# Performance work log

Measured on AMD Instinct MI355X. Metric: run time of the kernel, lower is better.

The kernel has to match this reference:

```python
import jax, jax.numpy as jnp
import numpy as np

# dims per module source / chosen globals
B, LB = 4, 28            # new frames, buffered frames; M = B+LB = L = 32
DK, DV = 256, 32         # Dk=256 hardcoded; Dv = 4*len_of_lookup+4 with len_of_lookup=7
HS, WS = 64, 64          # H//8, W//8 with H=W=512
LMAX = 32                # memory cap L
TRAIN_SZ = 1000          # log base train_sz
ALPHA = 0.5              # blend coefficient (original inits 0, which zeroes the branch)
# log(L*h*w + h*w, train_sz) / sqrt(Dk)
SCALE = float(np.log(LMAX * HS * WS + HS * WS) / np.log(TRAIN_SZ) / np.sqrt(DK))


def _xavier(key, fan_in, fan_out):
    lim = np.sqrt(6.0 / (fan_in + fan_out))
    return jax.random.uniform(key, (fan_in, fan_out), jnp.float32, -lim, lim)


def setup_inputs() -> dict:
    key = jax.random.key(0)
    ks = jax.random.split(key, 7)
    return {
        "fc": jax.random.normal(ks[0], (B, DK, HS, WS), jnp.float32),
        "fm": jax.random.normal(ks[1], (B, DV, HS, WS), jnp.float32),
        "key_buffer": jax.random.normal(ks[2], (LB, DK, HS, WS), jnp.float32),
        "value_buffer": jax.random.normal(ks[3], (LB, DV, HS, WS), jnp.float32),
        "Q": _xavier(ks[4], DK, DK),
        "K": _xavier(ks[5], DK, DK),
        "V": _xavier(ks[6], DV, DV),
    }


def reference(fc, fm, key_buffer, value_buffer, Q, K, V):
    # matmul = einsum('ijkl,jm->imkl'): per-pixel channel mixing
    q = jnp.einsum('bdhw,de->behw', fc, Q)                      # [B,Dk,h,w]
    k = jnp.concatenate([jnp.einsum('bdhw,de->behw', fc, K), key_buffer], axis=0)    # [M,Dk,h,w]
    v = jnp.concatenate([jnp.einsum('bdhw,de->behw', fm, V), value_buffer], axis=0)  # [M,Dv,h,w]
    # current_batch (=1) < L, so no slicing of k/v on this step
    scores = SCALE * jnp.einsum('bdhw,mdhw->bmhw', q, k)        # [B,M,h,w]
    attn = jax.nn.softmax(scores, axis=-1)                      # NOTE: softmax over width axis, as in source (dim=-1)
    ctx = jnp.einsum('bmhw,mdhw->bdhw', attn, v)                # [B,Dv,h,w]
    return fm + ALPHA * ctx
```

## Files before the change

kernel.cpp:

```cpp
#include <hip/hip_runtime.h>
#include <hip/hip_bf16.h>
#include <cmath>

#define NB 4
#define NM 32
#define DKc 256
#define DVc 32
#define NP 4096

using bf16x8 = __attribute__((ext_vector_type(8))) short;
using f32x4  = __attribute__((ext_vector_type(4))) float;
using f32x2  = __attribute__((ext_vector_type(2))) float;

__device__ __forceinline__ unsigned short f2bf(float f) {
    union { float f; unsigned u; } x; x.f = f;
    unsigned r = 0x7FFFu + ((x.u >> 16) & 1u);
    return (unsigned short)((x.u + r) >> 16);
}

__global__ __launch_bounds__(256) void k_prep(
    const float* __restrict__ fc, unsigned short* __restrict__ fcT,
    const float* __restrict__ Q, unsigned short* __restrict__ WTq,
    const float* __restrict__ K, unsigned short* __restrict__ WTk,
    const float* __restrict__ fm, const float* __restrict__ V, float* __restrict__ vproj) {
    int x = blockIdx.x;
    int t = threadIdx.x;
    if (x < 1056) {
        __shared__ float tile[64][65];
        const float* s; unsigned short* d; int R, C, r0, c0;
        if (x < 1024) {
            int bb = x >> 8, rest = x & 255;
            R = 256; C = 4096;
            r0 = (rest >> 6) * 64; c0 = (rest & 63) * 64;
            s = fc + (long)bb * 256 * 4096; d = fcT + (long)bb * 256 * 4096;
        } else {
            int i = x - 1024;
            int mat = i >> 4, idx = i & 15;
            R = 256; C = 256;
            r0 = (idx >> 2) * 64; c0 = (idx & 3) * 64;
            s = mat ? K : Q; d = mat ? WTk : WTq;
        }
        #pragma unroll
        for (int j = 0; j < 16; ++j) {
            int i = t + 256 * j;
            int r = i >> 6, c = i & 63;
            tile[r][c] = s[(long)(r0 + r) * C + c0 + c];
        }
        __syncthreads();
        #pragma unroll
        for (int j = 0; j < 8; ++j) {
            int i = t + 256 * j;
            int row = i >> 5;
            int pr = i & 31;
            float f0 = tile[2 * pr][row];
            float f1 = tile[2 * pr + 1][row];
            unsigned pack = (unsigned)f2bf(f0) | ((unsigned)f2bf(f1) << 16);
            reinterpret_cast<unsigned*>(d)[(((long)(c0 + row) * R + r0) >> 1) + pr] = pack;
        }
    } else {
        __shared__ float Vl[32][32];
        __shared__ float fml[32][256];
        int i = x - 1056;
        int b = i >> 4, p0 = (i & 15) * 256;
        #pragma unroll
        for (int j = 0; j < 4; ++j) { int ii = t + 256 * j; Vl[ii >> 5][ii & 31] = V[ii]; }
        for (int j = 0; j < 32; ++j) {
            int ii = t + 256 * j;
            int dd = ii >> 8, c = ii & 255;
            fml[dd][c] = fm[((long)b * DVc + dd) * NP + p0 + c];
        }
        __syncthreads();
        float acc[32];
        #pragma unroll
        for (int e = 0; e < 32; ++e) acc[e] = 0.f;
        for (int dd = 0; dd < 32; ++dd) {
            float fv = fml[dd][t];
            #pragma unroll
            for (int e = 0; e < 32; ++e) acc[e] += fv * Vl[dd][e];
        }
        #pragma unroll
        for (int e = 0; e < 32; ++e) vproj[((long)b * DVc + e) * NP + p0 + t] = acc[e];
    }
}

__global__ __launch_bounds__(256) void k_proj(
    const unsigned short* __restrict__ WTq, const unsigned short* __restrict__ WTk,
    const unsigned short* __restrict__ fcT,
    float* __restrict__ qproj, float* __restrict__ kproj) {
    int t = threadIdx.x;
    int wave = t >> 6, lane = t & 63;
    int y = blockIdx.y;
    int b = y & 3, mat = y >> 2;
    int p0 = blockIdx.x * 64;
    int ln = lane & 15, quad = lane >> 4;
    const unsigned short* WT = mat ? WTk : WTq;
    float* dst = mat ? kproj : qproj;
    int e0w = wave * 64;
    const unsigned short* bbase = fcT + ((long)b * NP + p0 + ln) * DKc + quad * 8;
    f32x4 acc[4][4] = {};
    for (int kk = 0; kk < DKc; kk += 32) {
        bf16x8 a[4], bb[4];
        #pragma unroll
        for (int i = 0; i < 4; ++i)
            a[i] = *reinterpret_cast<const bf16x8*>(WT + (long)(e0w + i * 16 + ln) * DKc + quad * 8 + kk);
        #pragma unroll
        for (int j = 0; j < 4; ++j)
            bb[j] = *reinterpret_cast<const bf16x8*>(bbase + (long)j * 16 * DKc + kk);
        #pragma unroll
        for (int i = 0; i < 4; ++i)
            #pragma unroll
            for (int j = 0; j < 4; ++j)
                acc[i][j] = __builtin_amdgcn_mfma_f32_16x16x32_bf16(a[i], bb[j], acc[i][j], 0, 0, 0);
    }
    #pragma unroll
    for (int i = 0; i < 4; ++i)
        #pragma unroll
        for (int j = 0; j < 4; ++j)
            #pragma unroll
            for (int r = 0; r < 4; ++r) {
                int e = e0w + i * 16 + quad * 4 + r, p = p0 + j * 16 + ln;
                dst[((long)b * DKc + e) * NP + p] = acc[i][j][r];
            }
}

__global__ __launch_bounds__(1024) void k_fused(
    const float* __restrict__ qproj, const float* __restrict__ kproj,
    const float* __restrict__ kbuf, const float* __restrict__ vproj,
    const float* __restrict__ vbuf, const float* __restrict__ fm,
    float* __restrict__ out, float scale) {
    __shared__ float smem[256 * 64];
    int t = threadIdx.x;
    int b = blockIdx.x >> 6, hrow = blockIdx.x & 63;
    int p0 = hrow * 64;
    int wave = t >> 6, lane = t & 63;

    {
        const float* qbase = qproj + (long)b * DKc * NP + p0;
        #pragma unroll
        for (int j = 0; j < 16; ++j) {
            int i = t + 1024 * j;
            int e = i >> 6, w = i & 63;
            smem[e * 64 + w] = qbase[(long)e * NP + w];
        }
    }
    __syncthreads();

    float attnw[2];
    {
        const float* kp[2];
        #pragma unroll
        for (int mi = 0; mi < 2; ++mi) {
            int m = wave * 2 + mi;
            kp[mi] = (m < 4 ? kproj + (long)m * DKc * NP : kbuf + (long)(m - 4) * DKc * NP)
                     + p0 + lane;
        }
        float s[2] = {0.f, 0.f};
        for (int e8 = 0; e8 < 256; e8 += 8) {
            float qv[8], kv[8][2];
            #pragma unroll
            for (int u = 0; u < 8; ++u) qv[u] = smem[(e8 + u) * 64 + lane];
            #pragma unroll
            for (int u = 0; u < 8; ++u)
                #pragma unroll
                for (int mi = 0; mi < 2; ++mi)
                    kv[u][mi] = kp[mi][(long)u * NP];
            #pragma unroll
            for (int u = 0; u < 8; ++u)
                #pragma unroll
                for (int mi = 0; mi < 2; ++mi)
                    s[mi] += qv[u] * kv[u][mi];
            #pragma unroll
            for (int mi = 0; mi < 2; ++mi) kp[mi] += 8 * NP;
        }
        #pragma unroll
        for (int mi = 0; mi < 2; ++mi) {
            float x = s[mi] * scale;
            float mx = x;
            #pragma unroll
            for (int d = 1; d < 64; d <<= 1) mx = fmaxf(mx, __shfl_xor(mx, d));
            float ev = __expf(x - mx);
            float sum = ev;
            #pragma unroll
            for (int d = 1; d < 64; d <<= 1) sum += __shfl_xor(sum, d);
            attnw[mi] = ev / sum;
        }
    }
    __syncthreads();
    #pragma unroll
    for (int mi = 0; mi < 2; ++mi)
        smem[(wave * 2 + mi) * 68 + lane] = attnw[mi];
    __syncthreads();

    {
        int dg = t >> 6, w = t & 63;
        float c2[2] = {0.f, 0.f};
        #pragma unroll
        for (int m = 0; m < NM; ++m) {
            float a = smem[m * 68 + w];
            const float* vp = (m < 4 ? vproj + (long)m * DVc * NP : vbuf + (long)(m - 4) * DVc * NP)
                              + (long)(dg * 2) * NP + p0 + w;
            #pragma unroll
            for (int i = 0; i < 2; ++i) c2[i] += a * vp[(long)i * NP];
        }
        #pragma unroll
        for (int i = 0; i < 2; ++i) {
            long gi = ((long)b * DVc + dg * 2 + i) * NP + p0 + w;
            out[gi] = fm[gi] + 0.5f * c2[i];
        }
    }
}

extern "C" void kernel_launch(void* const* d_in, const int* in_sizes, int n_in,
                              void* d_out, int out_size, void* d_ws, size_t ws_size,
                              hipStream_t stream) {
    const float* fc = (const float*)d_in[0];
    const float* fm = (const float*)d_in[1];
    const float* kb = (const float*)d_in[2];
    const float* vb = (const float*)d_in[3];
    const float* Q  = (const float*)d_in[4];
    const float* K  = (const float*)d_in[5];
    const float* V  = (const float*)d_in[6];
    float* out = (float*)d_out;
    char* ws = (char*)d_ws;
    float*          qproj = (float*)(ws);
    float*          kproj = (float*)(ws + 16777216);
    float*          vproj = (float*)(ws + 33554432);
    unsigned short* fcT   = (unsigned short*)(ws + 35651584);
    unsigned short* WTq   = (unsigned short*)(ws + 44040192);
    unsigned short* WTk   = (unsigned short*)(ws + 44171264);
    float scale = (float)(log(135168.0) / log(1000.0) / 16.0);

    hipLaunchKernelGGL(k_prep, dim3(1120), dim3(256), 0, stream,
                       fc, fcT, Q, WTq, K, WTk, fm, V, vproj);
    hipLaunchKernelGGL(k_proj, dim3(64, 8), dim3(256), 0, stream,
                       WTq, WTk, fcT, qproj, kproj);
    hipLaunchKernelGGL(k_fused, dim3(256), dim3(1024), 0, stream,
                       qproj, kproj, kb, vproj, vb, fm, out, scale);
}
```

Before: 252.6 us.

## Vectorize fused attention loads and split reductions across waves; halve proj pixel tile

The fused kernel now loads keys, queries and values as float4 per lane and splits the Dk reduction (and the memory-slot reduction for context) across two wave halves, combining the partial sums through shared memory. This aims to cut global load instruction count and raise memory-level parallelism on the bandwidth-heavy key-buffer read. The projection kernel's pixel tile drops from 64 to 32 with twice the grid, giving more blocks at the cost of reloading weights more often. It adds extra syncs and shared-memory round trips.

```diff
diff --git a/kernel.cpp b/kernel.cpp
--- a/kernel.cpp
+++ b/kernel.cpp
@@ -91,31 +91,31 @@
     int wave = t >> 6, lane = t & 63;
     int y = blockIdx.y;
     int b = y & 3, mat = y >> 2;
-    int p0 = blockIdx.x * 64;
+    int p0 = blockIdx.x * 32;
     int ln = lane & 15, quad = lane >> 4;
     const unsigned short* WT = mat ? WTk : WTq;
     float* dst = mat ? kproj : qproj;
     int e0w = wave * 64;
     const unsigned short* bbase = fcT + ((long)b * NP + p0 + ln) * DKc + quad * 8;
-    f32x4 acc[4][4] = {};
+    f32x4 acc[4][2] = {};
     for (int kk = 0; kk < DKc; kk += 32) {
-        bf16x8 a[4], bb[4];
+        bf16x8 a[4], bb[2];
         #pragma unroll
         for (int i = 0; i < 4; ++i)
             a[i] = *reinterpret_cast<const bf16x8*>(WT + (long)(e0w + i * 16 + ln) * DKc + quad * 8 + kk);
         #pragma unroll
-        for (int j = 0; j < 4; ++j)
+        for (int j = 0; j < 2; ++j)
             bb[j] = *reinterpret_cast<const bf16x8*>(bbase + (long)j * 16 * DKc + kk);
         #pragma unroll
         for (int i = 0; i < 4; ++i)
             #pragma unroll
-            for (int j = 0; j < 4; ++j)
+            for (int j = 0; j < 2; ++j)
                 acc[i][j] = __builtin_amdgcn_mfma_f32_16x16x32_bf16(a[i], bb[j], acc[i][j], 0, 0, 0);
     }
     #pragma unroll
     for (int i = 0; i < 4; ++i)
         #pragma unroll
-        for (int j = 0; j < 4; ++j)
+        for (int j = 0; j < 2; ++j)
             #pragma unroll
             for (int r = 0; r < 4; ++r) {
                 int e = e0w + i * 16 + quad * 4 + r, p = p0 + j * 16 + ln;
@@ -128,85 +128,91 @@
     const float* __restrict__ kbuf, const float* __restrict__ vproj,
     const float* __restrict__ vbuf, const float* __restrict__ fm,
     float* __restrict__ out, float scale) {
-    __shared__ float smem[256 * 64];
+    __shared__ float smem[16384];
     int t = threadIdx.x;
     int b = blockIdx.x >> 6, hrow = blockIdx.x & 63;
     int p0 = hrow * 64;
     int wave = t >> 6, lane = t & 63;
+    int wg = lane & 15;
 
     {
         const float* qbase = qproj + (long)b * DKc * NP + p0;
         #pragma unroll
-        for (int j = 0; j < 16; ++j) {
+        for (int j = 0; j < 4; ++j) {
             int i = t + 1024 * j;
-            int e = i >> 6, w = i & 63;
-            smem[e * 64 + w] = qbase[(long)e * NP + w];
-        }
-    }
-    __syncthreads();
-
-    float attnw[2];
+            int e = i >> 4, g = i & 15;
+            *reinterpret_cast<f32x4*>(&smem[e * 64 + g * 4]) =
+                *reinterpret_cast<const f32x4*>(qbase + (long)e * NP + g * 4);
+        }
+    }
+    __syncthreads();
+
     {
-        const float* kp[2];
-        #pragma unroll
-        for (int mi = 0; mi < 2; ++mi) {
-            int m = wave * 2 + mi;
-            kp[mi] = (m < 4 ? kproj + (long)m * DKc * NP : kbuf + (long)(m - 4) * DKc * NP)
-                     + p0 + lane;
-        }
-        float s[2] = {0.f, 0.f};
-        for (int e8 = 0; e8 < 256; e8 += 8) {
-            float qv[8], kv[8][2];
-            #pragma unroll
-            for (int u = 0; u < 8; ++u) qv[u] = smem[(e8 + u) * 64 + lane];
+        int mi = lane >> 4;
+        int eh = wave >> 3, mq = wave & 7;
+        int m = mq * 4 + mi;
+        const float* kbase = (mq == 0 ? kproj + (long)m * DKc * NP
+                                      : kbuf + (long)(m - 4) * DKc * NP)
+                             + (long)(eh * 128) * NP + p0 + wg * 4;
+        const float* qb = &smem[(eh * 128) * 64 + wg * 4];
+        f32x4 s4 = {0.f, 0.f, 0.f, 0.f};
+        for (int e8 = 0; e8 < 128; e8 += 8) {
+            f32x4 kv[8], qv[8];
             #pragma unroll
             for (int u = 0; u < 8; ++u)
-                #pragma unroll
-                for (int mi = 0; mi < 2; ++mi)
-                    kv[u][mi] = kp[mi][(long)u * NP];
+                kv[u] = *reinterpret_cast<const f32x4*>(kbase + (long)(e8 + u) * NP);
             #pragma unroll
             for (int u = 0; u < 8; ++u)
-                #pragma unroll
-                for (int mi = 0; mi < 2; ++mi)
-                    s[mi] += qv[u] * kv[u][mi];
-            #pragma unroll
-            for (int mi = 0; mi < 2; ++mi) kp[mi] += 8 * NP;
-        }
-        #pragma unroll
-        for (int mi = 0; mi < 2; ++mi) {
-            float x = s[mi] * scale;
-            float mx = x;
-            #pragma unroll
-            for (int d = 1; d < 64; d <<= 1) mx = fmaxf(mx, __shfl_xor(mx, d));
-            float ev = __expf(x - mx);
-            float sum = ev;
-            #pragma unroll
-            for (int d = 1; d < 64; d <<= 1) sum += __shfl_xor(sum, d);
-            attnw[mi] = ev / sum;
-        }
-    }
-    __syncthreads();
+                qv[u] = *reinterpret_cast<const f32x4*>(qb + (e8 + u) * 64);
+            #pragma unroll
+            for (int u = 0; u < 8; ++u)
+                s4 += qv[u] * kv[u];
+        }
+        __syncthreads();
+        *reinterpret_cast<f32x4*>(&smem[eh * 2048 + m * 64 + wg * 4]) = s4;
+    }
+    __syncthreads();
+
     #pragma unroll
-    for (int mi = 0; mi < 2; ++mi)
-        smem[(wave * 2 + mi) * 68 + lane] = attnw[mi];
+    for (int r = 0; r < 2; ++r) {
+        int m = wave * 2 + r;
+        float x = (smem[m * 64 + lane] + smem[2048 + m * 64 + lane]) * scale;
+        float mx = x;
+        #pragma unroll
+        for (int dd = 1; dd < 64; dd <<= 1) mx = fmaxf(mx, __shfl_xor(mx, dd));
+        float ev = __expf(x - mx);
+        float sum = ev;
+        #pragma unroll
+        for (int dd = 1; dd < 64; dd <<= 1) sum += __shfl_xor(sum, dd);
+        smem[4096 + m * 64 + lane] = ev / sum;
+    }
     __syncthreads();
 
     {
-        int dg = t >> 6, w = t & 63;
-        float c2[2] = {0.f, 0.f};
-        #pragma unroll
-        for (int m = 0; m < NM; ++m) {
-            float a = smem[m * 68 + w];
-            const float* vp = (m < 4 ? vproj + (long)m * DVc * NP : vbuf + (long)(m - 4) * DVc * NP)
-                              + (long)(dg * 2) * NP + p0 + w;
-            #pragma unroll
-            for (int i = 0; i < 2; ++i) c2[i] += a * vp[(long)i * NP];
-        }
-        #pragma unroll
-        for (int i = 0; i < 2; ++i) {
-            long gi = ((long)b * DVc + dg * 2 + i) * NP + p0 + w;
-            out[gi] = fm[gi] + 0.5f * c2[i];
-        }
+        int di = lane >> 4;
+        int mh = wave >> 3, dq = wave & 7;
+        int dd = dq * 4 + di;
+        f32x4 c4 = {0.f, 0.f, 0.f, 0.f};
+        #pragma unroll
+        for (int mm = 0; mm < 16; ++mm) {
+            int m = mh * 16 + mm;
+            const float* vb_ = (m < 4 ? vproj + (long)m * DVc * NP
+                                      : vbuf + (long)(m - 4) * DVc * NP);
+            f32x4 a4 = *reinterpret_cast<const f32x4*>(&smem[4096 + m * 64 + wg * 4]);
+            f32x4 v4 = *reinterpret_cast<const f32x4*>(vb_ + (long)dd * NP + p0 + wg * 4);
+            c4 += a4 * v4;
+        }
+        *reinterpret_cast<f32x4*>(&smem[mh * 2048 + dd * 64 + wg * 4]) = c4;
+    }
+    __syncthreads();
+
+    #pragma unroll
+    for (int r = 0; r < 2; ++r) {
+        int i = t + 1024 * r;
+        int dd = i >> 6, w = i & 63;
+        float c = smem[dd * 64 + w] + smem[2048 + dd * 64 + w];
+        long gi = ((long)b * DVc + dd) * NP + p0 + w;
+        out[gi] = fm[gi] + 0.5f * c;
     }
 }
 
@@ -232,7 +238,7 @@
 
     hipLaunchKernelGGL(k_prep, dim3(1120), dim3(256), 0, stream,
                        fc, fcT, Q, WTq, K, WTk, fm, V, vproj);
-    hipLaunchKernelGGL(k_proj, dim3(64, 8), dim3(256), 0, stream,
+    hipLaunchKernelGGL(k_proj, dim3(128, 8), dim3(256), 0, stream,
                        WTq, WTk, fcT, qproj, kproj);
     hipLaunchKernelGGL(k_fused, dim3(256), dim3(1024), 0, stream,
                        qproj, kproj, kb, vproj, vb, fm, out, scale);
```

Result: slower. 261.2 us (+3.4%).
